# Optimization experiments

Hardware: AMD Instinct MI355X
Metric: run time of the kernel (lower is better)

Reference implementation:

```python
import jax, jax.numpy as jnp
import numpy as np

D_K = 128
SCALE = 1.0 / np.sqrt(D_K).astype(np.float32)


def setup_inputs() -> dict:
    key = jax.random.key(0)
    kq, kk, kv = jax.random.split(key, 3)
    B, S, D = 8, 2048, D_K
    Q = jax.random.normal(kq, (B, S, D), dtype=jnp.float32)
    K = jax.random.normal(kk, (B, S, D), dtype=jnp.float32)
    V = jax.random.normal(kv, (B, S, D), dtype=jnp.float32)
    # causal mask: 1 = attend, 0 = block (per docstring semantics)
    mask = jnp.tril(jnp.ones((S, S), dtype=jnp.int32))
    return {"Q": Q, "K": K, "V": V, "mask": mask}


def reference(Q, K, V, mask):
    # scores: (B, S, S)
    scores = jnp.einsum("bqd,bkd->bqk", Q, K) * SCALE
    scores = jnp.where(mask == 0, -jnp.inf, scores)
    attention_weights = jax.nn.softmax(scores, axis=-1)
    output = jnp.einsum("bqk,bkd->bqd", attention_weights, V)
    return (output, attention_weights)
```

## Files before the change

### kernel.cpp

```cpp
#include <hip/hip_runtime.h>
#include <stdint.h>

#define BATCH 8
#define SEQ 2048
#define DH 128
#define QT 32
#define KT 64
#define NZ 32

static constexpr float SCALE_F = 0.08838834764831843f;

using bf16x8 = __attribute__((ext_vector_type(8))) short;
using f32x4  = __attribute__((ext_vector_type(4))) float;

__device__ inline unsigned short f2bf(float f) {
  unsigned u = __float_as_uint(f);
  u += 0x7fff + ((u >> 16) & 1);
  return (unsigned short)(u >> 16);
}

extern "C" __global__ void __launch_bounds__(256)
convert_qk(const float4* __restrict__ Q, const float4* __restrict__ K,
           ushort4* __restrict__ Qb, ushort4* __restrict__ Kb) {
  int i = blockIdx.x * 256 + threadIdx.x;
  float4 q = Q[i];
  float4 k = K[i];
  ushort4 uq, uk;
  uq.x = f2bf(q.x); uq.y = f2bf(q.y); uq.z = f2bf(q.z); uq.w = f2bf(q.w);
  uk.x = f2bf(k.x); uk.y = f2bf(k.y); uk.z = f2bf(k.z); uk.w = f2bf(k.w);
  Qb[i] = uq;
  Kb[i] = uk;
}

extern "C" __global__ void __launch_bounds__(256)
convert_v(const float* __restrict__ V, unsigned short* __restrict__ Vt) {
  __shared__ __align__(16) unsigned short L[DH][72];
  const int b = blockIdx.x >> 5;
  const int st = blockIdx.x & 31;
  const int s0 = st * 64;
  const int tid = threadIdx.x;
  const float* Vb = V + ((size_t)b * SEQ + s0) * DH;
#pragma unroll
  for (int it = 0; it < 8; ++it) {
    int f = (it * 256 + tid) * 4;
    int r = f >> 7, d0 = f & 127;
    float4 v = *(const float4*)(Vb + f);
    L[d0 + 0][r] = f2bf(v.x);
    L[d0 + 1][r] = f2bf(v.y);
    L[d0 + 2][r] = f2bf(v.z);
    L[d0 + 3][r] = f2bf(v.w);
  }
  __syncthreads();
  const int d = tid >> 1, h = tid & 1;
  unsigned short* dst = Vt + ((size_t)b * DH + d) * SEQ + s0 + h * 32;
  const uint4* src = (const uint4*)&L[d][h * 32];
#pragma unroll
  for (int j = 0; j < 4; ++j) ((uint4*)dst)[j] = src[j];
}

template <bool WS>
__global__ __launch_bounds__(256, 2) void attn_mfma(
    const float* __restrict__ Qg, const float* __restrict__ Kg,
    const float* __restrict__ Vg,
    const unsigned short* __restrict__ Qbf, const unsigned short* __restrict__ Kbf,
    const unsigned short* __restrict__ Vtg,
    float* __restrict__ Og, float* __restrict__ Wg) {
  __shared__ __align__(16) unsigned short Qs[QT][136];
  __shared__ __align__(16) unsigned short Ks[KT][136];
  __shared__ __align__(16) unsigned short Vs[DH][72];
  __shared__ __align__(16) unsigned short Ps[QT][72];
  __shared__ float red[4][QT];

  const int tid = threadIdx.x;
  const int lane = tid & 63;
  const int w = tid >> 6;
  const int l15 = lane & 15;
  const int quad = lane >> 4;

  const int b = blockIdx.x >> 5;
  const int z = blockIdx.x & 31;

  const float* Qgb = Qg + (size_t)b * SEQ * DH;
  const float* Kgb = Kg + (size_t)b * SEQ * DH;
  const float* Vgb = Vg + (size_t)b * SEQ * DH;
  const unsigned short* Qbb = Qbf + (size_t)b * SEQ * DH;
  const unsigned short* Kbb = Kbf + (size_t)b * SEQ * DH;
  const unsigned short* Vtb = Vtg + (size_t)b * DH * SEQ;
  float* Ob = Og + (size_t)b * SEQ * DH;
  float* Wb = Wg + (size_t)b * SEQ * SEQ;

  auto stageK = [&](int k0) {
    if constexpr (WS) {
#pragma unroll
      for (int it = 0; it < 4; ++it) {
        int f = (it * 256 + tid) * 8;
        int r = f >> 7, d0 = f & 127;
        *(uint4*)&Ks[r][d0] = *(const uint4*)(Kbb + (size_t)(k0 + r) * DH + d0);
      }
    } else {
#pragma unroll
      for (int it = 0; it < 8; ++it) {
        int f = (it * 256 + tid) * 4;
        int r = f >> 7, d0 = f & 127;
        float4 v = *(const float4*)(Kgb + (size_t)(k0 + r) * DH + d0);
        ushort4 u;
        u.x = f2bf(v.x); u.y = f2bf(v.y); u.z = f2bf(v.z); u.w = f2bf(v.w);
        *(ushort4*)&Ks[r][d0] = u;
      }
    }
  };
  auto stageV = [&](int k0) {
    if constexpr (WS) {
#pragma unroll
      for (int it = 0; it < 4; ++it) {
        int f = (it * 256 + tid) * 8;
        int d = f >> 6, s0 = f & 63;
        *(uint4*)&Vs[d][s0] = *(const uint4*)(Vtb + (size_t)d * SEQ + k0 + s0);
      }
    } else {
#pragma unroll
      for (int it = 0; it < 8; ++it) {
        int f = (it * 256 + tid) * 4;
        int r = f >> 7, d0 = f & 127;
        float4 v = *(const float4*)(Vgb + (size_t)(k0 + r) * DH + d0);
        Vs[d0 + 0][r] = f2bf(v.x);
        Vs[d0 + 1][r] = f2bf(v.y);
        Vs[d0 + 2][r] = f2bf(v.z);
        Vs[d0 + 3][r] = f2bf(v.w);
      }
    }
  };

  const int tiles[2] = {z, 63 - z};
  for (int ti = 0; ti < 2; ++ti) {
    const int t = tiles[ti];
    const int q0 = t * QT;
    const int ntk = t / 2 + 1;

    {
      const int c0f = ntk * KT;
      const int len = SEQ - c0f;
      if (len > 0) {
        const float4 z4 = {0.f, 0.f, 0.f, 0.f};
        for (int r = 0; r < QT; ++r) {
          float* row = Wb + (size_t)(q0 + r) * SEQ + c0f;
          for (int c = tid * 4; c < len; c += 1024) *(float4*)(row + c) = z4;
        }
      }
    }

    __syncthreads();
    if constexpr (WS) {
#pragma unroll
      for (int it = 0; it < 2; ++it) {
        int f = (it * 256 + tid) * 8;
        int r = f >> 7, d0 = f & 127;
        *(uint4*)&Qs[r][d0] = *(const uint4*)(Qbb + (size_t)(q0 + r) * DH + d0);
      }
    } else {
#pragma unroll
      for (int it = 0; it < 4; ++it) {
        int f = (it * 256 + tid) * 4;
        int r = f >> 7, d0 = f & 127;
        float4 v = *(const float4*)(Qgb + (size_t)(q0 + r) * DH + d0);
        ushort4 u;
        u.x = f2bf(v.x); u.y = f2bf(v.y); u.z = f2bf(v.z); u.w = f2bf(v.w);
        *(ushort4*)&Qs[r][d0] = u;
      }
    }

    float rs0[4] = {0.f, 0.f, 0.f, 0.f};
    float rs1[4] = {0.f, 0.f, 0.f, 0.f};
    for (int kt = 0; kt < ntk; ++kt) {
      __syncthreads();
      stageK(kt * KT);
      __syncthreads();
      f32x4 a0 = {0.f, 0.f, 0.f, 0.f};
      f32x4 a1 = {0.f, 0.f, 0.f, 0.f};
#pragma unroll
      for (int ks = 0; ks < 4; ++ks) {
        bf16x8 qa0 = *(const bf16x8*)&Qs[l15][ks * 32 + quad * 8];
        bf16x8 qa1 = *(const bf16x8*)&Qs[16 + l15][ks * 32 + quad * 8];
        bf16x8 kb = *(const bf16x8*)&Ks[w * 16 + l15][ks * 32 + quad * 8];
        a0 = __builtin_amdgcn_mfma_f32_16x16x32_bf16(qa0, kb, a0, 0, 0, 0);
        a1 = __builtin_amdgcn_mfma_f32_16x16x32_bf16(qa1, kb, a1, 0, 0, 0);
      }
      const int kcol = kt * KT + w * 16 + l15;
#pragma unroll
      for (int r = 0; r < 4; ++r) {
        const int row0 = q0 + quad * 4 + r;
        const int row1 = row0 + 16;
        rs0[r] += (kcol <= row0) ? __expf(a0[r] * SCALE_F) : 0.f;
        rs1[r] += (kcol <= row1) ? __expf(a1[r] * SCALE_F) : 0.f;
      }
    }
#pragma unroll
    for (int m = 1; m <= 8; m <<= 1) {
#pragma unroll
      for (int r = 0; r < 4; ++r) {
        rs0[r] += __shfl_xor(rs0[r], m);
        rs1[r] += __shfl_xor(rs1[r], m);
      }
    }
    __syncthreads();
    if (l15 == 0) {
#pragma unroll
      for (int r = 0; r < 4; ++r) {
        red[w][quad * 4 + r] = rs0[r];
        red[w][16 + quad * 4 + r] = rs1[r];
      }
    }
    __syncthreads();
    float inv0[4], inv1[4];
#pragma unroll
    for (int r = 0; r < 4; ++r) {
      float s0 = red[0][quad * 4 + r] + red[1][quad * 4 + r] +
                 red[2][quad * 4 + r] + red[3][quad * 4 + r];
      float s1 = red[0][16 + quad * 4 + r] + red[1][16 + quad * 4 + r] +
                 red[2][16 + quad * 4 + r] + red[3][16 + quad * 4 + r];
      inv0[r] = 1.f / s0;
      inv1[r] = 1.f / s1;
    }

    f32x4 o00 = {0.f, 0.f, 0.f, 0.f}, o01 = {0.f, 0.f, 0.f, 0.f};
    f32x4 o10 = {0.f, 0.f, 0.f, 0.f}, o11 = {0.f, 0.f, 0.f, 0.f};
    for (int kt = 0; kt < ntk; ++kt) {
      __syncthreads();
      stageK(kt * KT);
      stageV(kt * KT);
      __syncthreads();
      f32x4 a0 = {0.f, 0.f, 0.f, 0.f};
      f32x4 a1 = {0.f, 0.f, 0.f, 0.f};
#pragma unroll
      for (int ks = 0; ks < 4; ++ks) {
        bf16x8 qa0 = *(const bf16x8*)&Qs[l15][ks * 32 + quad * 8];
        bf16x8 qa1 = *(const bf16x8*)&Qs[16 + l15][ks * 32 + quad * 8];
        bf16x8 kb = *(const bf16x8*)&Ks[w * 16 + l15][ks * 32 + quad * 8];
        a0 = __builtin_amdgcn_mfma_f32_16x16x32_bf16(qa0, kb, a0, 0, 0, 0);
        a1 = __builtin_amdgcn_mfma_f32_16x16x32_bf16(qa1, kb, a1, 0, 0, 0);
      }
      const int kcol = kt * KT + w * 16 + l15;
#pragma unroll
      for (int r = 0; r < 4; ++r) {
        const int row0 = q0 + quad * 4 + r;
        const int row1 = row0 + 16;
        float p0 = (kcol <= row0) ? __expf(a0[r] * SCALE_F) * inv0[r] : 0.f;
        float p1 = (kcol <= row1) ? __expf(a1[r] * SCALE_F) * inv1[r] : 0.f;
        Wb[(size_t)row0 * SEQ + kcol] = p0;
        Wb[(size_t)row1 * SEQ + kcol] = p1;
        Ps[quad * 4 + r][w * 16 + l15] = f2bf(p0);
        Ps[16 + quad * 4 + r][w * 16 + l15] = f2bf(p1);
      }
      __syncthreads();
#pragma unroll
      for (int ks = 0; ks < 2; ++ks) {
        bf16x8 pa0 = *(const bf16x8*)&Ps[l15][ks * 32 + quad * 8];
        bf16x8 pa1 = *(const bf16x8*)&Ps[16 + l15][ks * 32 + quad * 8];
        bf16x8 v0 = *(const bf16x8*)&Vs[w * 32 + l15][ks * 32 + quad * 8];
        bf16x8 v1 = *(const bf16x8*)&Vs[w * 32 + 16 + l15][ks * 32 + quad * 8];
        o00 = __builtin_amdgcn_mfma_f32_16x16x32_bf16(pa0, v0, o00, 0, 0, 0);
        o01 = __builtin_amdgcn_mfma_f32_16x16x32_bf16(pa0, v1, o01, 0, 0, 0);
        o10 = __builtin_amdgcn_mfma_f32_16x16x32_bf16(pa1, v0, o10, 0, 0, 0);
        o11 = __builtin_amdgcn_mfma_f32_16x16x32_bf16(pa1, v1, o11, 0, 0, 0);
      }
    }
#pragma unroll
    for (int r = 0; r < 4; ++r) {
      const int row0 = q0 + quad * 4 + r;
      const int row1 = row0 + 16;
      Ob[(size_t)row0 * DH + w * 32 + l15] = o00[r];
      Ob[(size_t)row0 * DH + w * 32 + 16 + l15] = o01[r];
      Ob[(size_t)row1 * DH + w * 32 + l15] = o10[r];
      Ob[(size_t)row1 * DH + w * 32 + 16 + l15] = o11[r];
    }
  }
}

extern "C" void kernel_launch(void* const* d_in, const int* in_sizes, int n_in,
                              void* d_out, int out_size, void* d_ws, size_t ws_size,
                              hipStream_t stream) {
  const float* Q = (const float*)d_in[0];
  const float* K = (const float*)d_in[1];
  const float* V = (const float*)d_in[2];
  float* Out = (float*)d_out;
  float* W = Out + (size_t)BATCH * SEQ * DH;

  const size_t nel = (size_t)BATCH * SEQ * DH;
  const size_t need = nel * 2 * 3;
  if (ws_size >= need) {
    unsigned short* Qbf = (unsigned short*)d_ws;
    unsigned short* Kbf = Qbf + nel;
    unsigned short* Vt = Kbf + nel;
    hipLaunchKernelGGL(convert_qk, dim3((unsigned)(nel / 4 / 256)), dim3(256), 0, stream,
                       (const float4*)Q, (const float4*)K, (ushort4*)Qbf, (ushort4*)Kbf);
    hipLaunchKernelGGL(convert_v, dim3(BATCH * (SEQ / 64)), dim3(256), 0, stream, V, Vt);
    hipLaunchKernelGGL((attn_mfma<true>), dim3(BATCH * NZ), dim3(256), 0, stream,
                       Q, K, V, Qbf, Kbf, Vt, Out, W);
  } else {
    hipLaunchKernelGGL((attn_mfma<false>), dim3(BATCH * NZ), dim3(256), 0, stream,
                       Q, K, V, (const unsigned short*)nullptr,
                       (const unsigned short*)nullptr, (const unsigned short*)nullptr,
                       Out, W);
  }
}
```

Before: 232.1 us.

## Add software-pipelined attention kernel with double-buffered K and one block per tile

Replaces the workspace path with a new kernel that launches one block per 32-row query tile (512 blocks instead of 256 blocks that each handled a paired tile). It prefetches K and V tiles into registers two and one iterations ahead, double-buffers K in shared memory, and uses one barrier per iteration in the sum pass. The goal is to hide global load latency and to spread work across more blocks, at the cost of more registers and shared memory, and launches ordered longest-first without z/63-z pairing.

```diff
diff --git a/kernel.cpp b/kernel.cpp
--- a/kernel.cpp
+++ b/kernel.cpp
@@ -6,7 +6,6 @@
 #define DH 128
 #define QT 32
 #define KT 64
-#define NZ 32
 
 static constexpr float SCALE_F = 0.08838834764831843f;
 
@@ -58,13 +57,215 @@
   for (int j = 0; j < 4; ++j) ((uint4*)dst)[j] = src[j];
 }
 
-template <bool WS>
-__global__ __launch_bounds__(256, 2) void attn_mfma(
-    const float* __restrict__ Qg, const float* __restrict__ Kg,
-    const float* __restrict__ Vg,
+__global__ __launch_bounds__(256, 2) void attn_pipe(
     const unsigned short* __restrict__ Qbf, const unsigned short* __restrict__ Kbf,
     const unsigned short* __restrict__ Vtg,
     float* __restrict__ Og, float* __restrict__ Wg) {
+  __shared__ __align__(16) unsigned short Ks[2][KT][136];
+  __shared__ __align__(16) unsigned short Vs[DH][72];
+  __shared__ __align__(16) unsigned short Qs[QT][136];
+  __shared__ __align__(16) unsigned short Ps[QT][72];
+  __shared__ float red[4][QT];
+
+  const int tid = threadIdx.x;
+  const int lane = tid & 63;
+  const int w = tid >> 6;
+  const int l15 = lane & 15;
+  const int quad = lane >> 4;
+
+  const int b = blockIdx.x & 7;
+  const int t = 63 - (blockIdx.x >> 3);
+  const int q0 = t * QT;
+  const int ntk = t / 2 + 1;
+
+  const unsigned short* Qbb = Qbf + (size_t)b * SEQ * DH;
+  const unsigned short* Kbb = Kbf + (size_t)b * SEQ * DH;
+  const unsigned short* Vtb = Vtg + (size_t)b * DH * SEQ;
+  float* Ob = Og + (size_t)b * SEQ * DH;
+  float* Wb = Wg + (size_t)b * SEQ * SEQ;
+
+  {
+    const int c0f = ntk * KT;
+    const int len = SEQ - c0f;
+    if (len > 0) {
+      const float4 z4 = {0.f, 0.f, 0.f, 0.f};
+      for (int r = 0; r < QT; ++r) {
+        float* row = Wb + (size_t)(q0 + r) * SEQ + c0f;
+        for (int c = tid * 4; c < len; c += 1024) *(float4*)(row + c) = z4;
+      }
+    }
+  }
+
+#pragma unroll
+  for (int it = 0; it < 2; ++it) {
+    int f = (it * 256 + tid) * 8;
+    int r = f >> 7, d0 = f & 127;
+    *(uint4*)&Qs[r][d0] = *(const uint4*)(Qbb + (size_t)(q0 + r) * DH + d0);
+  }
+
+  uint4 ka[4], kn[4], va[4], vn[4];
+
+  auto loadK = [&](uint4* dst, int k0) {
+#pragma unroll
+    for (int it = 0; it < 4; ++it) {
+      int f = (it * 256 + tid) * 8;
+      int r = f >> 7, d0 = f & 127;
+      dst[it] = *(const uint4*)(Kbb + (size_t)(k0 + r) * DH + d0);
+    }
+  };
+  auto writeK = [&](const uint4* src, int buf) {
+#pragma unroll
+    for (int it = 0; it < 4; ++it) {
+      int f = (it * 256 + tid) * 8;
+      int r = f >> 7, d0 = f & 127;
+      *(uint4*)&Ks[buf][r][d0] = src[it];
+    }
+  };
+  auto loadV = [&](uint4* dst, int k0) {
+#pragma unroll
+    for (int it = 0; it < 4; ++it) {
+      int f = (it * 256 + tid) * 8;
+      int d = f >> 6, s0 = f & 63;
+      dst[it] = *(const uint4*)(Vtb + (size_t)d * SEQ + k0 + s0);
+    }
+  };
+  auto writeV = [&](const uint4* src) {
+#pragma unroll
+    for (int it = 0; it < 4; ++it) {
+      int f = (it * 256 + tid) * 8;
+      int d = f >> 6, s0 = f & 63;
+      *(uint4*)&Vs[d][s0] = src[it];
+    }
+  };
+
+  loadK(ka, 0);
+  writeK(ka, 0);
+  if (ntk > 1) loadK(ka, KT);
+  __syncthreads();
+
+  float rs0[4] = {0.f, 0.f, 0.f, 0.f};
+  float rs1[4] = {0.f, 0.f, 0.f, 0.f};
+  for (int kt = 0; kt < ntk; ++kt) {
+    if (kt + 2 < ntk) loadK(kn, (kt + 2) * KT);
+    const int cur = kt & 1;
+    f32x4 a0 = {0.f, 0.f, 0.f, 0.f};
+    f32x4 a1 = {0.f, 0.f, 0.f, 0.f};
+#pragma unroll
+    for (int ks = 0; ks < 4; ++ks) {
+      bf16x8 qa0 = *(const bf16x8*)&Qs[l15][ks * 32 + quad * 8];
+      bf16x8 qa1 = *(const bf16x8*)&Qs[16 + l15][ks * 32 + quad * 8];
+      bf16x8 kb = *(const bf16x8*)&Ks[cur][w * 16 + l15][ks * 32 + quad * 8];
+      a0 = __builtin_amdgcn_mfma_f32_16x16x32_bf16(qa0, kb, a0, 0, 0, 0);
+      a1 = __builtin_amdgcn_mfma_f32_16x16x32_bf16(qa1, kb, a1, 0, 0, 0);
+    }
+    const int kcol = kt * KT + w * 16 + l15;
+#pragma unroll
+    for (int r = 0; r < 4; ++r) {
+      const int row0 = q0 + quad * 4 + r;
+      const int row1 = row0 + 16;
+      rs0[r] += (kcol <= row0) ? __expf(a0[r] * SCALE_F) : 0.f;
+      rs1[r] += (kcol <= row1) ? __expf(a1[r] * SCALE_F) : 0.f;
+    }
+    if (kt + 1 < ntk) writeK(ka, 1 - cur);
+    __syncthreads();
+#pragma unroll
+    for (int j = 0; j < 4; ++j) ka[j] = kn[j];
+  }
+
+#pragma unroll
+  for (int m = 1; m <= 8; m <<= 1) {
+#pragma unroll
+    for (int r = 0; r < 4; ++r) {
+      rs0[r] += __shfl_xor(rs0[r], m);
+      rs1[r] += __shfl_xor(rs1[r], m);
+    }
+  }
+  if (l15 == 0) {
+#pragma unroll
+    for (int r = 0; r < 4; ++r) {
+      red[w][quad * 4 + r] = rs0[r];
+      red[w][16 + quad * 4 + r] = rs1[r];
+    }
+  }
+  __syncthreads();
+  float inv0[4], inv1[4];
+#pragma unroll
+  for (int r = 0; r < 4; ++r) {
+    float s0 = red[0][quad * 4 + r] + red[1][quad * 4 + r] +
+               red[2][quad * 4 + r] + red[3][quad * 4 + r];
+    float s1 = red[0][16 + quad * 4 + r] + red[1][16 + quad * 4 + r] +
+               red[2][16 + quad * 4 + r] + red[3][16 + quad * 4 + r];
+    inv0[r] = 1.f / s0;
+    inv1[r] = 1.f / s1;
+  }
+
+  loadK(ka, 0);
+  loadV(va, 0);
+  writeK(ka, 0);
+  if (ntk > 1) loadK(ka, KT);
+  __syncthreads();
+
+  f32x4 o00 = {0.f, 0.f, 0.f, 0.f}, o01 = {0.f, 0.f, 0.f, 0.f};
+  f32x4 o10 = {0.f, 0.f, 0.f, 0.f}, o11 = {0.f, 0.f, 0.f, 0.f};
+  for (int kt = 0; kt < ntk; ++kt) {
+    if (kt + 2 < ntk) loadK(kn, (kt + 2) * KT);
+    if (kt + 1 < ntk) loadV(vn, (kt + 1) * KT);
+    const int cur = kt & 1;
+    f32x4 a0 = {0.f, 0.f, 0.f, 0.f};
+    f32x4 a1 = {0.f, 0.f, 0.f, 0.f};
+#pragma unroll
+    for (int ks = 0; ks < 4; ++ks) {
+      bf16x8 qa0 = *(const bf16x8*)&Qs[l15][ks * 32 + quad * 8];
+      bf16x8 qa1 = *(const bf16x8*)&Qs[16 + l15][ks * 32 + quad * 8];
+      bf16x8 kb = *(const bf16x8*)&Ks[cur][w * 16 + l15][ks * 32 + quad * 8];
+      a0 = __builtin_amdgcn_mfma_f32_16x16x32_bf16(qa0, kb, a0, 0, 0, 0);
+      a1 = __builtin_amdgcn_mfma_f32_16x16x32_bf16(qa1, kb, a1, 0, 0, 0);
+    }
+    const int kcol = kt * KT + w * 16 + l15;
+#pragma unroll
+    for (int r = 0; r < 4; ++r) {
+      const int row0 = q0 + quad * 4 + r;
+      const int row1 = row0 + 16;
+      float p0 = (kcol <= row0) ? __expf(a0[r] * SCALE_F) * inv0[r] : 0.f;
+      float p1 = (kcol <= row1) ? __expf(a1[r] * SCALE_F) * inv1[r] : 0.f;
+      Wb[(size_t)row0 * SEQ + kcol] = p0;
+      Wb[(size_t)row1 * SEQ + kcol] = p1;
+      Ps[quad * 4 + r][w * 16 + l15] = f2bf(p0);
+      Ps[16 + quad * 4 + r][w * 16 + l15] = f2bf(p1);
+    }
+    writeV(va);
+    if (kt + 1 < ntk) writeK(ka, 1 - cur);
+    __syncthreads();
+#pragma unroll
+    for (int ks = 0; ks < 2; ++ks) {
+      bf16x8 pa0 = *(const bf16x8*)&Ps[l15][ks * 32 + quad * 8];
+      bf16x8 pa1 = *(const bf16x8*)&Ps[16 + l15][ks * 32 + quad * 8];
+      bf16x8 v0 = *(const bf16x8*)&Vs[w * 32 + l15][ks * 32 + quad * 8];
+      bf16x8 v1 = *(const bf16x8*)&Vs[w * 32 + 16 + l15][ks * 32 + quad * 8];
+      o00 = __builtin_amdgcn_mfma_f32_16x16x32_bf16(pa0, v0, o00, 0, 0, 0);
+      o01 = __builtin_amdgcn_mfma_f32_16x16x32_bf16(pa0, v1, o01, 0, 0, 0);
+      o10 = __builtin_amdgcn_mfma_f32_16x16x32_bf16(pa1, v0, o10, 0, 0, 0);
+      o11 = __builtin_amdgcn_mfma_f32_16x16x32_bf16(pa1, v1, o11, 0, 0, 0);
+    }
+    __syncthreads();
+#pragma unroll
+    for (int j = 0; j < 4; ++j) { ka[j] = kn[j]; va[j] = vn[j]; }
+  }
+
+#pragma unroll
+  for (int r = 0; r < 4; ++r) {
+    const int row0 = q0 + quad * 4 + r;
+    const int row1 = row0 + 16;
+    Ob[(size_t)row0 * DH + w * 32 + l15] = o00[r];
+    Ob[(size_t)row0 * DH + w * 32 + 16 + l15] = o01[r];
+    Ob[(size_t)row1 * DH + w * 32 + l15] = o10[r];
+    Ob[(size_t)row1 * DH + w * 32 + 16 + l15] = o11[r];
+  }
+}
+
+__global__ __launch_bounds__(256, 2) void attn_fb(
+    const float* __restrict__ Qg, const float* __restrict__ Kg,
+    const float* __restrict__ Vg, float* __restrict__ Og, float* __restrict__ Wg) {
   __shared__ __align__(16) unsigned short Qs[QT][136];
   __shared__ __align__(16) unsigned short Ks[KT][136];
   __shared__ __align__(16) unsigned short Vs[DH][72];
@@ -83,51 +284,30 @@
   const float* Qgb = Qg + (size_t)b * SEQ * DH;
   const float* Kgb = Kg + (size_t)b * SEQ * DH;
   const float* Vgb = Vg + (size_t)b * SEQ * DH;
-  const unsigned short* Qbb = Qbf + (size_t)b * SEQ * DH;
-  const unsigned short* Kbb = Kbf + (size_t)b * SEQ * DH;
-  const unsigned short* Vtb = Vtg + (size_t)b * DH * SEQ;
   float* Ob = Og + (size_t)b * SEQ * DH;
   float* Wb = Wg + (size_t)b * SEQ * SEQ;
 
   auto stageK = [&](int k0) {
-    if constexpr (WS) {
-#pragma unroll
-      for (int it = 0; it < 4; ++it) {
-        int f = (it * 256 + tid) * 8;
-        int r = f >> 7, d0 = f & 127;
-        *(uint4*)&Ks[r][d0] = *(const uint4*)(Kbb + (size_t)(k0 + r) * DH + d0);
-      }
-    } else {
-#pragma unroll
-      for (int it = 0; it < 8; ++it) {
-        int f = (it * 256 + tid) * 4;
-        int r = f >> 7, d0 = f & 127;
-        float4 v = *(const float4*)(Kgb + (size_t)(k0 + r) * DH + d0);
-        ushort4 u;
-        u.x = f2bf(v.x); u.y = f2bf(v.y); u.z = f2bf(v.z); u.w = f2bf(v.w);
-        *(ushort4*)&Ks[r][d0] = u;
-      }
+#pragma unroll
+    for (int it = 0; it < 8; ++it) {
+      int f = (it * 256 + tid) * 4;
+      int r = f >> 7, d0 = f & 127;
+      float4 v = *(const float4*)(Kgb + (size_t)(k0 + r) * DH + d0);
+      ushort4 u;
+      u.x = f2bf(v.x); u.y = f2bf(v.y); u.z = f2bf(v.z); u.w = f2bf(v.w);
+      *(ushort4*)&Ks[r][d0] = u;
     }
   };
   auto stageV = [&](int k0) {
-    if constexpr (WS) {
-#pragma unroll
-      for (int it = 0; it < 4; ++it) {
-        int f = (it * 256 + tid) * 8;
-        int d = f >> 6, s0 = f & 63;
-        *(uint4*)&Vs[d][s0] = *(const uint4*)(Vtb + (size_t)d * SEQ + k0 + s0);
-      }
-    } else {
-#pragma unroll
-      for (int it = 0; it < 8; ++it) {
-        int f = (it * 256 + tid) * 4;
-        int r = f >> 7, d0 = f & 127;
-        float4 v = *(const float4*)(Vgb + (size_t)(k0 + r) * DH + d0);
-        Vs[d0 + 0][r] = f2bf(v.x);
-        Vs[d0 + 1][r] = f2bf(v.y);
-        Vs[d0 + 2][r] = f2bf(v.z);
-        Vs[d0 + 3][r] = f2bf(v.w);
-      }
+#pragma unroll
+    for (int it = 0; it < 8; ++it) {
+      int f = (it * 256 + tid) * 4;
+      int r = f >> 7, d0 = f & 127;
+      float4 v = *(const float4*)(Vgb + (size_t)(k0 + r) * DH + d0);
+      Vs[d0 + 0][r] = f2bf(v.x);
+      Vs[d0 + 1][r] = f2bf(v.y);
+      Vs[d0 + 2][r] = f2bf(v.z);
+      Vs[d0 + 3][r] = f2bf(v.w);
     }
   };
 
@@ -136,7 +316,6 @@
     const int t = tiles[ti];
     const int q0 = t * QT;
     const int ntk = t / 2 + 1;
-
     {
       const int c0f = ntk * KT;
       const int len = SEQ - c0f;
@@ -148,27 +327,16 @@
         }
       }
     }
-
-    __syncthreads();
-    if constexpr (WS) {
-#pragma unroll
-      for (int it = 0; it < 2; ++it) {
-        int f = (it * 256 + tid) * 8;
-        int r = f >> 7, d0 = f & 127;
-        *(uint4*)&Qs[r][d0] = *(const uint4*)(Qbb + (size_t)(q0 + r) * DH + d0);
-      }
-    } else {
-#pragma unroll
-      for (int it = 0; it < 4; ++it) {
-        int f = (it * 256 + tid) * 4;
-        int r = f >> 7, d0 = f & 127;
-        float4 v = *(const float4*)(Qgb + (size_t)(q0 + r) * DH + d0);
-        ushort4 u;
-        u.x = f2bf(v.x); u.y = f2bf(v.y); u.z = f2bf(v.z); u.w = f2bf(v.w);
-        *(ushort4*)&Qs[r][d0] = u;
-      }
-    }
-
+    __syncthreads();
+#pragma unroll
+    for (int it = 0; it < 4; ++it) {
+      int f = (it * 256 + tid) * 4;
+      int r = f >> 7, d0 = f & 127;
+      float4 v = *(const float4*)(Qgb + (size_t)(q0 + r) * DH + d0);
+      ushort4 u;
+      u.x = f2bf(v.x); u.y = f2bf(v.y); u.z = f2bf(v.z); u.w = f2bf(v.w);
+      *(ushort4*)&Qs[r][d0] = u;
+    }
     float rs0[4] = {0.f, 0.f, 0.f, 0.f};
     float rs1[4] = {0.f, 0.f, 0.f, 0.f};
     for (int kt = 0; kt < ntk; ++kt) {
@@ -221,7 +389,6 @@
       inv0[r] = 1.f / s0;
       inv1[r] = 1.f / s1;
     }
-
     f32x4 o00 = {0.f, 0.f, 0.f, 0.f}, o01 = {0.f, 0.f, 0.f, 0.f};
     f32x4 o10 = {0.f, 0.f, 0.f, 0.f}, o11 = {0.f, 0.f, 0.f, 0.f};
     for (int kt = 0; kt < ntk; ++kt) {
@@ -294,12 +461,10 @@
     hipLaunchKernelGGL(convert_qk, dim3((unsigned)(nel / 4 / 256)), dim3(256), 0, stream,
                        (const float4*)Q, (const float4*)K, (ushort4*)Qbf, (ushort4*)Kbf);
     hipLaunchKernelGGL(convert_v, dim3(BATCH * (SEQ / 64)), dim3(256), 0, stream, V, Vt);
-    hipLaunchKernelGGL((attn_mfma<true>), dim3(BATCH * NZ), dim3(256), 0, stream,
-                       Q, K, V, Qbf, Kbf, Vt, Out, W);
+    hipLaunchKernelGGL(attn_pipe, dim3(BATCH * 64), dim3(256), 0, stream,
+                       Qbf, Kbf, Vt, Out, W);
   } else {
-    hipLaunchKernelGGL((attn_mfma<false>), dim3(BATCH * NZ), dim3(256), 0, stream,
-                       Q, K, V, (const unsigned short*)nullptr,
-                       (const unsigned short*)nullptr, (const unsigned short*)nullptr,
-                       Out, W);
-  }
-}
+    hipLaunchKernelGGL(attn_fb, dim3(BATCH * 32), dim3(256), 0, stream,
+                       Q, K, V, Out, W);
+  }
+}
```

New measurement: 441.0 us. +90.0%, slower.
